# Kernel optimization log

Hardware: AMD Instinct MI355X
Metric: run time of the kernel (lower is better)

The kernel has to match this reference:

```python
import jax, jax.numpy as jnp
import numpy as np

B, CIN, D, H, W = 4, 512, 8, 28, 28
C = 128  # reduction_channel = 512 // 4
N = D * H * W


def setup_inputs() -> dict:
    key = jax.random.key(0)
    ks = jax.random.split(key, 9)
    s_in = 1.0 / np.sqrt(CIN)
    s_r = 1.0 / np.sqrt(C)
    return {
        "x": jax.random.normal(ks[0], (B, CIN, D, H, W), dtype=jnp.float32),
        "k_w": jax.random.normal(ks[1], (C, CIN), dtype=jnp.float32) * s_in,
        "k_b": jax.random.normal(ks[2], (C,), dtype=jnp.float32) * 0.01,
        "q_w": jax.random.normal(ks[3], (C, CIN), dtype=jnp.float32) * s_in,
        "q_b": jax.random.normal(ks[4], (C,), dtype=jnp.float32) * 0.01,
        "v_w": jax.random.normal(ks[5], (C, CIN), dtype=jnp.float32) * s_in,
        "v_b": jax.random.normal(ks[6], (C,), dtype=jnp.float32) * 0.01,
        "r_w": jax.random.normal(ks[7], (CIN, C), dtype=jnp.float32) * s_r,
        "r_b": jax.random.normal(ks[8], (CIN,), dtype=jnp.float32) * 0.01,
    }


def reference(x, k_w, k_b, q_w, q_b, v_w, v_b, r_w, r_b):
    b, cin, d, h, w = x.shape
    n = d * h * w
    xf = x.reshape(b, cin, n)  # [b, 512, N]

    # 1x1x1 convs == per-position linear; produce [b, N, C] directly (permuted)
    k = jnp.einsum('bcn,oc->bno', xf, k_w) + k_b  # [b, N, C]
    q = jnp.einsum('bcn,oc->bno', xf, q_w) + q_b
    v = jnp.einsum('bcn,oc->bno', xf, v_w) + v_b

    # w[b,i,j] = sum_d k[b,i,d] * q[b,j,d]
    attn = jnp.einsum('bid,bjd->bij', k, q)  # [b, N, N]
    scale = jnp.float32(1.0 / np.sqrt(n))
    # FAITHFUL quirk: original uses nn.Softmax(dim=0) -> softmax over BATCH axis
    attn = jax.nn.softmax(attn * scale, axis=0)

    out = jnp.einsum('bid,bdj->bij', attn, v)  # [b, N, C]
    out = out.transpose(0, 2, 1).reshape(b, C, d, h, w)  # [b, C, D, H, W]

    # restore 1x1x1 conv back to 512 channels
    of = out.reshape(b, C, n)
    res = jnp.einsum('bcn,oc->bon', of, r_w) + r_b[None, :, None]
    return res.reshape(b, cin, d, h, w)
```

## Files before the change

### kernel.cpp

```cpp
#include <hip/hip_runtime.h>
#include <cmath>

typedef __bf16 bf16;
typedef bf16 bf16x8 __attribute__((ext_vector_type(8)));
typedef bf16 bf16x4 __attribute__((ext_vector_type(4)));
typedef float f32x4 __attribute__((ext_vector_type(4)));

#define MFMA __builtin_amdgcn_mfma_f32_16x16x32_bf16

constexpr int BB  = 4;
constexpr int CIN = 512;
constexpr int CC  = 128;
constexpr int NN  = 6272;
constexpr int NT  = NN / 32;
constexpr int IT  = NN / 64;

__device__ __forceinline__ void glds16(const void* g, void* l) {
    __builtin_amdgcn_global_load_lds(
        (const __attribute__((address_space(1))) unsigned int*)g,
        (__attribute__((address_space(3))) unsigned int*)l, 16, 0, 0);
}
#define WAIT_LGKM0 asm volatile("s_waitcnt lgkmcnt(0)" ::: "memory")
#define WAIT_VM0   asm volatile("s_waitcnt vmcnt(0)" ::: "memory")
#define WAIT_VM8   asm volatile("s_waitcnt vmcnt(8)" ::: "memory")
#define SBAR()     do { __builtin_amdgcn_s_barrier(); __builtin_amdgcn_sched_barrier(0); } while (0)

__device__ __forceinline__ float hw_exp2(float x) {
    float r;
    asm("v_exp_f32 %0, %1" : "=v"(r) : "v"(x));
    return r;
}

__global__ __launch_bounds__(256) void k_wcvt(
    const float* __restrict__ kw, const float* __restrict__ qw,
    const float* __restrict__ vw, const float* __restrict__ rw,
    bf16* __restrict__ o)
{
    const int idx = (blockIdx.x * 256 + threadIdx.x) * 4;
    const float* s;
    if      (idx < 65536)  s = kw + idx;
    else if (idx < 131072) s = qw + (idx - 65536);
    else if (idx < 196608) s = vw + (idx - 131072);
    else                   s = rw + (idx - 196608);
    f32x4 v = *(const f32x4*)s;
    bf16* d = o + idx;
    d[0] = (bf16)v[0]; d[1] = (bf16)v[1]; d[2] = (bf16)v[2]; d[3] = (bf16)v[3];
}

__global__ __launch_bounds__(512, 2) void k_kqv(
    const float* __restrict__ x,
    const bf16* __restrict__ wkb, const float* __restrict__ kbias,
    const bf16* __restrict__ wqb, const float* __restrict__ qbias,
    const bf16* __restrict__ wvb, const float* __restrict__ vbias,
    bf16* __restrict__ Kg, bf16* __restrict__ Qg, bf16* __restrict__ Vt)
{
    __shared__ bf16 xt[64 * 512];
    const int b  = blockIdx.y;
    const int n0 = blockIdx.x * 64;
    const int t  = threadIdx.x;

    {
        const int nl = t & 63;
        const int cg = t >> 6;
        const float* xp = x + (size_t)b * CIN * NN + n0 + nl;
        for (int c0 = cg * 8; c0 < CIN; c0 += 64) {
            bf16x8 pk;
            #pragma unroll
            for (int j = 0; j < 8; ++j) pk[j] = (bf16)xp[(size_t)(c0 + j) * NN];
            const int blk = ((c0 >> 3) ^ (nl & 7));
            *(bf16x8*)(&xt[nl * 512 + (blk << 3)]) = pk;
        }
    }
    __syncthreads();

    const int w  = t >> 6;
    const int ln = t & 63;
    const int lr = ln & 15;
    const int lg = ln >> 4;

    {
        const int h  = w >> 2;
        const int op = w & 3;
        const bf16* pw = h ? wqb : wkb;
        const float* pb = h ? qbias : kbias;
        bf16* dst = h ? Qg : Kg;
        f32x4 acc[4][2];
        #pragma unroll
        for (int ns = 0; ns < 4; ++ns)
            #pragma unroll
            for (int oi = 0; oi < 2; ++oi) acc[ns][oi] = f32x4{0.f, 0.f, 0.f, 0.f};
        for (int kk = 0; kk < 16; ++kk) {
            bf16x8 bw[2];
            #pragma unroll
            for (int oi = 0; oi < 2; ++oi)
                bw[oi] = *(const bf16x8*)(&pw[(size_t)((op * 2 + oi) * 16 + lr) * CIN + (kk << 5) + (lg << 3)]);
            #pragma unroll
            for (int ns = 0; ns < 4; ++ns) {
                const int nrow = ns * 16 + lr;
                bf16x8 a = *(const bf16x8*)(&xt[nrow * 512 + ((((kk << 2) + lg) ^ (nrow & 7)) << 3)]);
                acc[ns][0] = MFMA(a, bw[0], acc[ns][0], 0, 0, 0);
                acc[ns][1] = MFMA(a, bw[1], acc[ns][1], 0, 0, 0);
            }
        }
        #pragma unroll
        for (int ns = 0; ns < 4; ++ns)
            #pragma unroll
            for (int oi = 0; oi < 2; ++oi)
                #pragma unroll
                for (int r = 0; r < 4; ++r) {
                    const int n_ = n0 + ns * 16 + (lg << 2) + r;
                    const int o  = (op * 2 + oi) * 16 + lr;
                    const int oe = h ? ((((o >> 3) ^ (n_ & 7)) << 3) | (o & 7)) : o;
                    dst[((size_t)b * NN + n_) * CC + oe] = (bf16)(acc[ns][oi][r] + pb[o]);
                }
    }

    {
        f32x4 vac[4];
        #pragma unroll
        for (int i = 0; i < 4; ++i) vac[i] = f32x4{0.f, 0.f, 0.f, 0.f};
        for (int kk = 0; kk < 16; ++kk) {
            bf16x8 a = *(const bf16x8*)(&wvb[(size_t)(w * 16 + lr) * CIN + (kk << 5) + (lg << 3)]);
            #pragma unroll
            for (int nt = 0; nt < 4; ++nt) {
                const int nrow = nt * 16 + lr;
                bf16x8 bfr = *(const bf16x8*)(&xt[nrow * 512 + ((((kk << 2) + lg) ^ (nrow & 7)) << 3)]);
                vac[nt] = MFMA(a, bfr, vac[nt], 0, 0, 0);
            }
        }
        #pragma unroll
        for (int nt = 0; nt < 4; ++nt)
            #pragma unroll
            for (int r = 0; r < 4; ++r) {
                const int o  = w * 16 + (lg << 2) + r;
                const int n_ = n0 + nt * 16 + lr;
                Vt[((size_t)b * CC + o) * NN + n_] = (bf16)(vac[nt][r] + vbias[o]);
            }
    }
}

__global__ __launch_bounds__(512, 2) void k_attn(
    const bf16* __restrict__ Kg, const bf16* __restrict__ Qg,
    const bf16* __restrict__ Vt, bf16* __restrict__ midp,
    int dch, int tpc, float scl2)
{
    extern __shared__ char smem[];
    bf16* Qs = (bf16*)smem;
    bf16* Ps = (bf16*)(smem + 65536);

    const int bid = blockIdx.x;
    const int dc  = bid / IT;
    const int i0  = (bid % IT) * 64;
    const int t   = threadIdx.x;
    const int w   = t >> 6, ln = t & 63, lr = ln & 15, lg = ln >> 4;

    const int t_lo = dc * tpc;
    const int t_hi = min(t_lo + tpc, NT);

    const char* qsrc[4];
    #pragma unroll
    for (int i = 0; i < 4; ++i) {
        const int row = ((w * 4 + i) << 2) + (ln >> 4);
        qsrc[i] = (const char*)Qg + (((size_t)(row >> 5) * NN + (row & 31)) * CC + (ln & 15) * 8) * 2;
    }
    auto stage = [&](int bf, int tile) {
        const size_t qoff = (size_t)tile * 8192;
        char* qb = smem + bf * 32768 + w * 4096;
        #pragma unroll
        for (int i = 0; i < 4; ++i) glds16(qsrc[i] + qoff, qb + i * 1024);
    };

    stage(0, t_lo);
    WAIT_VM0;
    SBAR();

    int buf = 0, pbuf = 0;

    if (w < 4) {
        const int ch = w & 1, iq = w >> 1;
        bf16x8 kf[2][4][4];
        #pragma unroll
        for (int ws2 = 0; ws2 < 2; ++ws2)
            #pragma unroll
            for (int b = 0; b < 4; ++b)
                #pragma unroll
                for (int kk = 0; kk < 4; ++kk)
                    kf[ws2][b][kk] = *(const bf16x8*)(&Kg[((size_t)b * NN + i0 + (iq * 2 + ws2) * 16 + lr) * CC + (kk << 5) + (lg << 3)]);

        const int d_  = ch * 16 + lr;
        const int dsw = lr & 7;

        for (int tt = t_lo; tt < t_hi; ++tt) {
            if (tt + 1 < t_hi) stage(buf ^ 1, tt + 1);
            __builtin_amdgcn_sched_barrier(0);

            bf16* Qb = Qs + buf * 16384;
            f32x4 sa[2][4];
            #pragma unroll
            for (int ws2 = 0; ws2 < 2; ++ws2)
                #pragma unroll
                for (int b = 0; b < 4; ++b) sa[ws2][b] = f32x4{0.f, 0.f, 0.f, 0.f};
            __builtin_amdgcn_s_setprio(1);
            #pragma unroll
            for (int b = 0; b < 4; ++b) {
                const int row = b * 32 + d_;
                #pragma unroll
                for (int kk = 0; kk < 4; ++kk) {
                    bf16x8 qf = *(const bf16x8*)(&Qb[row * 128 + ((((kk << 2) + lg) ^ dsw) << 3)]);
                    sa[0][b] = MFMA(qf, kf[0][b][kk], sa[0][b], 0, 0, 0);
                    sa[1][b] = MFMA(qf, kf[1][b][kk], sa[1][b], 0, 0, 0);
                }
            }
            __builtin_amdgcn_s_setprio(0);

            #pragma unroll
            for (int ws2 = 0; ws2 < 2; ++ws2) {
                float p[4][4];
                #pragma unroll
                for (int r = 0; r < 4; ++r) {
                    const float e0 = hw_exp2(sa[ws2][0][r] * scl2);
                    const float e1 = hw_exp2(sa[ws2][1][r] * scl2);
                    const float e2 = hw_exp2(sa[ws2][2][r] * scl2);
                    const float e3 = hw_exp2(sa[ws2][3][r] * scl2);
                    const float rs = __builtin_amdgcn_rcpf(e0 + e1 + e2 + e3);
                    p[0][r] = e0 * rs; p[1][r] = e1 * rs; p[2][r] = e2 * rs; p[3][r] = e3 * rs;
                }
                const int row  = (iq * 2 + ws2) * 16 + lr;
                const int colg = (ch << 1) | (lg >> 1);
                const int sub  = (lg & 1) << 2;
                #pragma unroll
                for (int b = 0; b < 4; ++b) {
                    const int rw_ = b * 64 + row;
                    bf16x4 pk;
                    pk[0] = (bf16)p[b][0]; pk[1] = (bf16)p[b][1];
                    pk[2] = (bf16)p[b][2]; pk[3] = (bf16)p[b][3];
                    *(bf16x4*)(&Ps[pbuf * 8192 + rw_ * 32 + ((colg ^ ((rw_ >> 1) & 3)) << 3) + sub]) = pk;
                }
            }

            WAIT_LGKM0;
            WAIT_VM0;
            SBAR();
            buf ^= 1; pbuf ^= 1;
        }
    } else {
        const int pb = w - 4;
        const bf16* vbase[8];
        #pragma unroll
        for (int ct = 0; ct < 8; ++ct)
            vbase[ct] = Vt + ((size_t)pb * CC + ct * 16 + lr) * NN + (lg << 3);

        f32x4 oacc[4][8];
        #pragma unroll
        for (int mt = 0; mt < 4; ++mt)
            #pragma unroll
            for (int ct = 0; ct < 8; ++ct) oacc[mt][ct] = f32x4{0.f, 0.f, 0.f, 0.f};

        bf16x8 vfp[8];
        for (int tt = t_lo; tt < t_hi; ++tt) {
            if (tt + 1 < t_hi) stage(buf ^ 1, tt + 1);
            __builtin_amdgcn_sched_barrier(0);

            if (tt > t_lo) {
                const bf16* Pr = Ps + (pbuf ^ 1) * 8192;
                bf16x8 pan[4];
                #pragma unroll
                for (int mt = 0; mt < 4; ++mt) {
                    const int prow = pb * 64 + mt * 16 + lr;
                    pan[mt] = *(const bf16x8*)(&Pr[prow * 32 + ((lg ^ ((prow >> 1) & 3)) << 3)]);
                }
                __builtin_amdgcn_s_setprio(1);
                #pragma unroll
                for (int mt = 0; mt < 4; ++mt)
                    #pragma unroll
                    for (int ct = 0; ct < 8; ++ct)
                        oacc[mt][ct] = MFMA(pan[mt], vfp[ct], oacc[mt][ct], 0, 0, 0);
                __builtin_amdgcn_s_setprio(0);
            }

            #pragma unroll
            for (int ct = 0; ct < 8; ++ct)
                vfp[ct] = *(const bf16x8*)(vbase[ct] + tt * 32);

            WAIT_LGKM0;
            WAIT_VM8;
            SBAR();
            buf ^= 1; pbuf ^= 1;
        }

        {
            const bf16* Pr = Ps + (pbuf ^ 1) * 8192;
            bf16x8 pan[4];
            #pragma unroll
            for (int mt = 0; mt < 4; ++mt) {
                const int prow = pb * 64 + mt * 16 + lr;
                pan[mt] = *(const bf16x8*)(&Pr[prow * 32 + ((lg ^ ((prow >> 1) & 3)) << 3)]);
            }
            #pragma unroll
            for (int mt = 0; mt < 4; ++mt)
                #pragma unroll
                for (int ct = 0; ct < 8; ++ct)
                    oacc[mt][ct] = MFMA(pan[mt], vfp[ct], oacc[mt][ct], 0, 0, 0);
        }

        #pragma unroll
        for (int mt = 0; mt < 4; ++mt)
            #pragma unroll
            for (int ct = 0; ct < 8; ++ct)
                #pragma unroll
                for (int r = 0; r < 4; ++r) {
                    const int n_ = i0 + mt * 16 + (lg << 2) + r;
                    const int c  = ct * 16 + lr;
                    midp[(((size_t)dc * 4 + pb) * NN + n_) * CC + c] = (bf16)oacc[mt][ct][r];
                }
    }
}

__global__ __launch_bounds__(512, 2) void k_out2(
    const bf16* __restrict__ midp, const bf16* __restrict__ rwb,
    const float* __restrict__ rb, float* __restrict__ out, int dch)
{
    __shared__ bf16 red[64 * 128];
    const int b  = blockIdx.y;
    const int n0 = blockIdx.x * 64;
    const int t  = threadIdx.x;
    const int w  = t >> 6, ln = t & 63, lr = ln & 15, lg = ln >> 4;

    const size_t dstride = (size_t)BB * NN * CC;

    #pragma unroll
    for (int j2 = 0; j2 < 2; ++j2) {
        const int j  = t * 2 + j2;
        const int n  = j >> 4;
        const int cg = j & 15;
        const bf16* mp = midp + ((size_t)b * NN + n0 + n) * CC + (cg << 3);
        float s[8] = {0.f, 0.f, 0.f, 0.f, 0.f, 0.f, 0.f, 0.f};
        for (int d = 0; d < dch; ++d) {
            bf16x8 v = *(const bf16x8*)(mp + (size_t)d * dstride);
            #pragma unroll
            for (int k = 0; k < 8; ++k) s[k] += (float)v[k];
        }
        bf16x8 o;
        #pragma unroll
        for (int k = 0; k < 8; ++k) o[k] = (bf16)s[k];
        *(bf16x8*)(&red[n * 128 + ((cg ^ (n & 7)) << 3)]) = o;
    }
    __syncthreads();

    f32x4 acc[4][4];
    #pragma unroll
    for (int mt = 0; mt < 4; ++mt)
        #pragma unroll
        for (int nt = 0; nt < 4; ++nt) acc[mt][nt] = f32x4{0.f, 0.f, 0.f, 0.f};

    for (int kk = 0; kk < 4; ++kk) {
        bf16x8 bfr[4];
        #pragma unroll
        for (int nt = 0; nt < 4; ++nt) {
            const int n_ = nt * 16 + lr;
            const int cg = (kk << 2) + lg;
            bfr[nt] = *(const bf16x8*)(&red[n_ * 128 + ((cg ^ (n_ & 7)) << 3)]);
        }
        #pragma unroll
        for (int mt = 0; mt < 4; ++mt) {
            const int o = w * 64 + mt * 16 + lr;
            bf16x8 af = *(const bf16x8*)(&rwb[(size_t)o * CC + (kk << 5) + (lg << 3)]);
            #pragma unroll
            for (int nt = 0; nt < 4; ++nt)
                acc[mt][nt] = MFMA(af, bfr[nt], acc[mt][nt], 0, 0, 0);
        }
    }
    #pragma unroll
    for (int mt = 0; mt < 4; ++mt)
        #pragma unroll
        for (int nt = 0; nt < 4; ++nt)
            #pragma unroll
            for (int r = 0; r < 4; ++r) {
                const int o  = w * 64 + mt * 16 + (lg << 2) + r;
                const int n_ = n0 + nt * 16 + lr;
                out[((size_t)b * CIN + o) * NN + n_] = acc[mt][nt][r] + rb[o];
            }
}

extern "C" void kernel_launch(void* const* d_in, const int* in_sizes, int n_in,
                              void* d_out, int out_size, void* d_ws, size_t ws_size,
                              hipStream_t stream)
{
    const float* x  = (const float*)d_in[0];
    const float* kw = (const float*)d_in[1];
    const float* kb = (const float*)d_in[2];
    const float* qw = (const float*)d_in[3];
    const float* qb = (const float*)d_in[4];
    const float* vw = (const float*)d_in[5];
    const float* vb = (const float*)d_in[6];
    const float* rw = (const float*)d_in[7];
    const float* rb = (const float*)d_in[8];
    float* out = (float*)d_out;

    const size_t szP = (size_t)BB * NN * CC;
    char* ws = (char*)d_ws;
    bf16* wkb = (bf16*)ws;
    bf16* wqb = wkb + 65536;
    bf16* wvb = wqb + 65536;
    bf16* rwb = wvb + 65536;
    bf16* Kg  = (bf16*)(ws + 524288);
    bf16* Qg  = Kg + szP;
    bf16* Vt  = Qg + szP;
    const size_t base = 524288 + 3 * szP * sizeof(bf16);
    bf16* midp = (bf16*)(ws + base);

    int dch = 1;
    if      (base + 5 * szP * sizeof(bf16) <= ws_size) dch = 5;
    else if (base + 4 * szP * sizeof(bf16) <= ws_size) dch = 4;
    else if (base + 2 * szP * sizeof(bf16) <= ws_size) dch = 2;

    const float scl2 = 1.4426950408889634f / sqrtf((float)NN);

    k_wcvt<<<dim3(256), 256, 0, stream>>>(kw, qw, vw, rw, wkb);

    k_kqv<<<dim3(IT, BB), 512, 0, stream>>>(x, wkb, kb, wqb, qb, wvb, vb, Kg, Qg, Vt);

    const int tpc = (NT + dch - 1) / dch;
    const size_t lds = 98304;
    (void)hipFuncSetAttribute((const void*)k_attn,
                              hipFuncAttributeMaxDynamicSharedMemorySize, (int)lds);
    k_attn<<<dim3(IT * dch), 512, lds, stream>>>(Kg, Qg, Vt, midp, dch, tpc, scl2);

    k_out2<<<dim3(IT, BB), 512, 0, stream>>>(midp, rwb, rb, out, dch);
}
```

Measured before the change: 197.0 us.

## Load Q tiles directly into registers instead of staging through LDS

The attention kernel stops staging Q tiles into shared memory with async global-to-LDS loads. Each score wave now prefetches its Q fragments for the next tile straight from global memory into registers, and the Q projection stores in an unswizzled layout to match. This frees 64KB of LDS and drops the vmcnt waits, which could allow more blocks per CU. In exchange, Q is loaded redundantly per wave with less coalescing, and register pressure rises.

```diff
diff --git a/kernel.cpp b/kernel.cpp
--- a/kernel.cpp
+++ b/kernel.cpp
@@ -15,14 +15,7 @@
 constexpr int NT  = NN / 32;
 constexpr int IT  = NN / 64;
 
-__device__ __forceinline__ void glds16(const void* g, void* l) {
-    __builtin_amdgcn_global_load_lds(
-        (const __attribute__((address_space(1))) unsigned int*)g,
-        (__attribute__((address_space(3))) unsigned int*)l, 16, 0, 0);
-}
 #define WAIT_LGKM0 asm volatile("s_waitcnt lgkmcnt(0)" ::: "memory")
-#define WAIT_VM0   asm volatile("s_waitcnt vmcnt(0)" ::: "memory")
-#define WAIT_VM8   asm volatile("s_waitcnt vmcnt(8)" ::: "memory")
 #define SBAR()     do { __builtin_amdgcn_s_barrier(); __builtin_amdgcn_sched_barrier(0); } while (0)
 
 __device__ __forceinline__ float hw_exp2(float x) {
@@ -110,8 +103,7 @@
                 for (int r = 0; r < 4; ++r) {
                     const int n_ = n0 + ns * 16 + (lg << 2) + r;
                     const int o  = (op * 2 + oi) * 16 + lr;
-                    const int oe = h ? ((((o >> 3) ^ (n_ & 7)) << 3) | (o & 7)) : o;
-                    dst[((size_t)b * NN + n_) * CC + oe] = (bf16)(acc[ns][oi][r] + pb[o]);
+                    dst[((size_t)b * NN + n_) * CC + o] = (bf16)(acc[ns][oi][r] + pb[o]);
                 }
     }
 
@@ -144,9 +136,7 @@
     const bf16* __restrict__ Vt, bf16* __restrict__ midp,
     int dch, int tpc, float scl2)
 {
-    extern __shared__ char smem[];
-    bf16* Qs = (bf16*)smem;
-    bf16* Ps = (bf16*)(smem + 65536);
+    __shared__ bf16 Ps[2 * 4 * 64 * 32];
 
     const int bid = blockIdx.x;
     const int dc  = bid / IT;
@@ -157,24 +147,7 @@
     const int t_lo = dc * tpc;
     const int t_hi = min(t_lo + tpc, NT);
 
-    const char* qsrc[4];
-    #pragma unroll
-    for (int i = 0; i < 4; ++i) {
-        const int row = ((w * 4 + i) << 2) + (ln >> 4);
-        qsrc[i] = (const char*)Qg + (((size_t)(row >> 5) * NN + (row & 31)) * CC + (ln & 15) * 8) * 2;
-    }
-    auto stage = [&](int bf, int tile) {
-        const size_t qoff = (size_t)tile * 8192;
-        char* qb = smem + bf * 32768 + w * 4096;
-        #pragma unroll
-        for (int i = 0; i < 4; ++i) glds16(qsrc[i] + qoff, qb + i * 1024);
-    };
-
-    stage(0, t_lo);
-    WAIT_VM0;
-    SBAR();
-
-    int buf = 0, pbuf = 0;
+    int pbuf = 0;
 
     if (w < 4) {
         const int ch = w & 1, iq = w >> 1;
@@ -187,14 +160,22 @@
                 for (int kk = 0; kk < 4; ++kk)
                     kf[ws2][b][kk] = *(const bf16x8*)(&Kg[((size_t)b * NN + i0 + (iq * 2 + ws2) * 16 + lr) * CC + (kk << 5) + (lg << 3)]);
 
-        const int d_  = ch * 16 + lr;
-        const int dsw = lr & 7;
+        const bf16* qbase[4];
+        #pragma unroll
+        for (int b = 0; b < 4; ++b)
+            qbase[b] = Qg + ((size_t)b * NN + ch * 16 + lr) * CC + (lg << 3);
+
+        bf16x8 qf[4][4];
+        {
+            const size_t qo = (size_t)t_lo * 32 * CC;
+            #pragma unroll
+            for (int b = 0; b < 4; ++b)
+                #pragma unroll
+                for (int kk = 0; kk < 4; ++kk)
+                    qf[b][kk] = *(const bf16x8*)(qbase[b] + qo + (kk << 5));
+        }
 
         for (int tt = t_lo; tt < t_hi; ++tt) {
-            if (tt + 1 < t_hi) stage(buf ^ 1, tt + 1);
-            __builtin_amdgcn_sched_barrier(0);
-
-            bf16* Qb = Qs + buf * 16384;
             f32x4 sa[2][4];
             #pragma unroll
             for (int ws2 = 0; ws2 < 2; ++ws2)
@@ -202,16 +183,22 @@
                 for (int b = 0; b < 4; ++b) sa[ws2][b] = f32x4{0.f, 0.f, 0.f, 0.f};
             __builtin_amdgcn_s_setprio(1);
             #pragma unroll
-            for (int b = 0; b < 4; ++b) {
-                const int row = b * 32 + d_;
+            for (int b = 0; b < 4; ++b)
                 #pragma unroll
                 for (int kk = 0; kk < 4; ++kk) {
-                    bf16x8 qf = *(const bf16x8*)(&Qb[row * 128 + ((((kk << 2) + lg) ^ dsw) << 3)]);
-                    sa[0][b] = MFMA(qf, kf[0][b][kk], sa[0][b], 0, 0, 0);
-                    sa[1][b] = MFMA(qf, kf[1][b][kk], sa[1][b], 0, 0, 0);
-                }
-            }
+                    sa[0][b] = MFMA(qf[b][kk], kf[0][b][kk], sa[0][b], 0, 0, 0);
+                    sa[1][b] = MFMA(qf[b][kk], kf[1][b][kk], sa[1][b], 0, 0, 0);
+                }
             __builtin_amdgcn_s_setprio(0);
+
+            if (tt + 1 < t_hi) {
+                const size_t qo = (size_t)(tt + 1) * 32 * CC;
+                #pragma unroll
+                for (int b = 0; b < 4; ++b)
+                    #pragma unroll
+                    for (int kk = 0; kk < 4; ++kk)
+                        qf[b][kk] = *(const bf16x8*)(qbase[b] + qo + (kk << 5));
+            }
 
             #pragma unroll
             for (int ws2 = 0; ws2 < 2; ++ws2) {
@@ -239,9 +226,8 @@
             }
 
             WAIT_LGKM0;
-            WAIT_VM0;
             SBAR();
-            buf ^= 1; pbuf ^= 1;
+            pbuf ^= 1;
         }
     } else {
         const int pb = w - 4;
@@ -258,9 +244,6 @@
 
         bf16x8 vfp[8];
         for (int tt = t_lo; tt < t_hi; ++tt) {
-            if (tt + 1 < t_hi) stage(buf ^ 1, tt + 1);
-            __builtin_amdgcn_sched_barrier(0);
-
             if (tt > t_lo) {
                 const bf16* Pr = Ps + (pbuf ^ 1) * 8192;
                 bf16x8 pan[4];
@@ -283,9 +266,8 @@
                 vfp[ct] = *(const bf16x8*)(vbase[ct] + tt * 32);
 
             WAIT_LGKM0;
-            WAIT_VM8;
             SBAR();
-            buf ^= 1; pbuf ^= 1;
+            pbuf ^= 1;
         }
 
         {
@@ -421,10 +403,7 @@
     k_kqv<<<dim3(IT, BB), 512, 0, stream>>>(x, wkb, kb, wqb, qb, wvb, vb, Kg, Qg, Vt);
 
     const int tpc = (NT + dch - 1) / dch;
-    const size_t lds = 98304;
-    (void)hipFuncSetAttribute((const void*)k_attn,
-                              hipFuncAttributeMaxDynamicSharedMemorySize, (int)lds);
-    k_attn<<<dim3(IT * dch), 512, lds, stream>>>(Kg, Qg, Vt, midp, dch, tpc, scl2);
+    k_attn<<<dim3(IT * dch), 512, 0, stream>>>(Kg, Qg, Vt, midp, dch, tpc, scl2);
 
     k_out2<<<dim3(IT, BB), 512, 0, stream>>>(midp, rwb, rb, out, dch);
 }
```

Measured after the change: 285.5 us. 44.9% more time.
